# Optimization experiments

Hardware: AMD Instinct MI355X
Metric: run time of the kernel (lower is better)

## Reference

```python
import jax, jax.numpy as jnp
import numpy as np

ALPHA_MGD = 2e-05
NOISE_SIGMA = 8.0
NOISE_VAR = NOISE_SIGMA ** 2  # 64.0


def _conv2d(x, w, b, pad):
    # x: [N,C,H,W], w: [O,I,kh,kw]
    y = jax.lax.conv_general_dilated(
        x, w, window_strides=(1, 1), padding=[(pad, pad), (pad, pad)],
        dimension_numbers=("NCHW", "OIHW", "NCHW"))
    return y + b[None, :, None, None]


def setup_inputs() -> dict:
    key = jax.random.key(0)
    ks = jax.random.split(key, 8)
    N, Cs, Ct, H, W = 8, 128, 256, 64, 64
    return {
        "preds_S": jax.random.normal(ks[0], (N, Cs, H, W), jnp.float32),
        "preds_T": jax.random.normal(ks[1], (N, Ct, H, W), jnp.float32),
        "W_align": jax.random.normal(ks[2], (Ct, Cs, 1, 1), jnp.float32) * 0.05,
        "b_align": jnp.zeros((Ct,), jnp.float32),
        "W_gen1": jax.random.normal(ks[3], (Ct, Ct, 3, 3), jnp.float32) * 0.02,
        "b_gen1": jnp.zeros((Ct,), jnp.float32),
        "W_gen2": jax.random.normal(ks[4], (Ct, Ct, 3, 3), jnp.float32) * 0.02,
        "b_gen2": jnp.zeros((Ct,), jnp.float32),
    }


def reference(preds_S, preds_T, W_align, b_align, W_gen1, b_gen1, W_gen2, b_gen2):
    # align student channels to teacher channels (1x1 conv)
    s = _conv2d(preds_S, W_align, b_align, pad=0)
    N, C, H, W = preds_T.shape
    # deterministic checkerboard mask: tile([[0,1],[1,0]]) cropped to HxW -> (h+w) % 2
    hh = jnp.arange(H)[:, None]
    ww = jnp.arange(W)[None, :]
    mat = ((hh + ww) % 2).astype(s.dtype)  # [H,W]
    masked_fea = s * mat  # broadcast over [N,C,H,W]
    # generation network: conv3x3 -> relu -> conv3x3
    new_fea = _conv2d(jax.nn.relu(_conv2d(masked_fea, W_gen1, b_gen1, pad=1)), W_gen2, b_gen2, pad=1)
    # bmc_loss_md(pred=preds_T, target=new_fea, noise_var=64):
    # logits[i,j] = MVN(pred_i, noise_var*I).log_prob(target_j); the normalization
    # constant is class-independent and cancels in cross-entropy, keep the quadratic term.
    p = preds_T.reshape(N, -1)   # [N, D], D = C*H*W
    t = new_fea.reshape(N, -1)   # [N, D]
    # pairwise squared L2 via ||p||^2 + ||t||^2 - 2 p.t  (avoids NxNxD blow-up)
    sq = (jnp.sum(p * p, axis=1)[:, None]
          + jnp.sum(t * t, axis=1)[None, :]
          - 2.0 * (p @ t.T))  # [N, N]
    logits = -0.5 * sq / NOISE_VAR
    # cross_entropy(logits, arange(N)) = mean_i (logsumexp_j logits[i,j] - logits[i,i])
    ce = jnp.mean(jax.nn.logsumexp(logits, axis=1) - jnp.diagonal(logits))
    loss = ce * (2.0 * NOISE_VAR) / N
    return loss * ALPHA_MGD
```

## Files before the change

### kernel.cpp

```cpp
#include <hip/hip_runtime.h>

typedef unsigned short u16;
typedef short short8 __attribute__((ext_vector_type(8)));
typedef unsigned short ushort8 __attribute__((ext_vector_type(8)));
typedef float floatx16 __attribute__((ext_vector_type(16)));

#define PLANE8   34848
#define NSTRIDE  1115136

__device__ __forceinline__ u16 f2b(float f) {
  unsigned u = __builtin_bit_cast(unsigned, f);
  return (u16)((u + 0x7FFFu + ((u >> 16) & 1u)) >> 16);
}
__device__ __forceinline__ float b2f(u16 b) {
  return __builtin_bit_cast(float, ((unsigned)b) << 16);
}

typedef const __attribute__((address_space(1))) unsigned int* gptr_t;
typedef __attribute__((address_space(3))) unsigned int* sptr_t;

__global__ __launch_bounds__(256) void kprep(
    const float* __restrict__ Wg1, u16* __restrict__ Wsw1,
    const float* __restrict__ Wg2, u16* __restrict__ Wsw2,
    const float* __restrict__ Wa,  u16* __restrict__ Wb,
    const float* __restrict__ pS,  u16* __restrict__ T,
    u16* __restrict__ masked, u16* __restrict__ t1)
{
  __shared__ u16 Ls[64 * 136];
  int b = blockIdx.x, t = threadIdx.x;

  if (b < 576) {
    const float* W = (b < 288) ? Wg1 : Wg2;
    u16* D = (b < 288) ? Wsw1 : Wsw2;
    int bb = (b < 288) ? b : b - 288;
    int cid = bb * 256 + t;
    int d = cid % 1152, ctcg = cid / 1152;
    int ct = ctcg & 3, cg = ctcg >> 2;
    int colow = d & 31, cihalf = (d >> 5) & 1, sc = (d >> 6) & 1, tap = d >> 7;
    int co = ct * 64 + sc * 32 + colow;
    short8 v;
    #pragma unroll
    for (int jj = 0; jj < 8; ++jj) {
      int ci = cg * 16 + cihalf * 8 + jj;
      v[jj] = (short)f2b(W[((size_t)(co * 256 + ci)) * 9 + tap]);
    }
    *(short8*)&D[(size_t)cid * 8] = v;
  } else if (b < 592) {
    int v = (b - 576) * 256 + t;
    int colow = v & 31, hfb = (v >> 5) & 1, cog = (v >> 6) & 7, k = v >> 9;
    int co = cog * 32 + colow;
    int ci0 = k * 16 + hfb * 8;
    float4 f0 = *(const float4*)(Wa + (size_t)co * 128 + ci0);
    float4 f1 = *(const float4*)(Wa + (size_t)co * 128 + ci0 + 4);
    short8 o;
    o[0] = (short)f2b(f0.x); o[1] = (short)f2b(f0.y);
    o[2] = (short)f2b(f0.z); o[3] = (short)f2b(f0.w);
    o[4] = (short)f2b(f1.x); o[5] = (short)f2b(f1.y);
    o[6] = (short)f2b(f1.z); o[7] = (short)f2b(f1.w);
    *(short8*)&Wb[(size_t)v * 8] = o;
  } else if (b < 1104) {
    int bb = b - 592;
    int n = bb >> 6, pt = bb & 63, pix0 = pt * 64;
    int ci = t >> 1, ph = t & 1;
    const float* src = pS + ((size_t)n * 128 + ci) * 4096 + pix0 + ph * 32;
    #pragma unroll
    for (int i = 0; i < 8; ++i) {
      float4 v4 = *(const float4*)(src + i * 4);
      int pix = ph * 32 + i * 4;
      Ls[(pix + 0) * 136 + ci] = f2b(v4.x);
      Ls[(pix + 1) * 136 + ci] = f2b(v4.y);
      Ls[(pix + 2) * 136 + ci] = f2b(v4.z);
      Ls[(pix + 3) * 136 + ci] = f2b(v4.w);
    }
    __syncthreads();
    int p = t >> 2, q = t & 3;
    const u16* row = Ls + p * 136 + q * 32;
    u16* dst = T + ((size_t)n * 4096 + pix0 + p) * 128 + q * 32;
    #pragma unroll
    for (int k2 = 0; k2 < 4; ++k2)
      *(ushort8*)(dst + k2 * 8) = *(const ushort8*)(row + k2 * 8);
  } else {
    int p = b - 1104;
    u16* base = ((p >> 8) ? t1 : masked);
    int q = p & 255;
    base += (size_t)(q >> 5) * NSTRIDE + (size_t)(q & 31) * PLANE8;
    short8 z;
    #pragma unroll
    for (int jj = 0; jj < 8; ++jj) z[jj] = 0;
    #pragma unroll
    for (int pass = 0; pass < 2; ++pass) {
      int seg = t + pass * 256;
      if (seg < 264) {
        int off;
        if (seg < 66)       off = seg * 8;
        else if (seg < 132) off = (65 * 66 + (seg - 66)) * 8;
        else if (seg < 198) off = ((seg - 132) * 66) * 8;
        else                off = ((seg - 198) * 66 + 65) * 8;
        *(short8*)(base + off) = z;
      }
    }
  }
}

__global__ __launch_bounds__(256) void k1m(const u16* __restrict__ T,
    const u16* __restrict__ Wb, const float* __restrict__ ba,
    u16* __restrict__ mk)
{
  __shared__ __align__(16) u16 Wl[32768];
  int b = blockIdx.x;
  int n = b >> 5, pt = b & 31;
  int t = threadIdx.x, wid = t >> 6, lane = t & 63;
  int ml = lane & 31, hf = lane >> 5;

  #pragma unroll
  for (int kk = 0; kk < 16; ++kk) {
    int chunk = kk * 256 + t;
    __builtin_amdgcn_global_load_lds((gptr_t)(const void*)(Wb + (size_t)chunk * 8),
                                     (sptr_t)(void*)(Wl + chunk * 8), 16, 0, 0);
  }

  const u16* Tn = T + (size_t)n * 524288;
  const u16* ap[4];
  #pragma unroll
  for (int g = 0; g < 4; ++g)
    ap[g] = Tn + (size_t)(pt * 128 + g * 32 + ml) * 128 + hf * 8;

  floatx16 acc[2][4];
  #pragma unroll
  for (int q = 0; q < 2; ++q)
    #pragma unroll
    for (int g = 0; g < 4; ++g)
      #pragma unroll
      for (int i = 0; i < 16; ++i) acc[q][g][i] = 0.f;

  __syncthreads();

  const short8* WlV = (const short8*)Wl;
  int cogb = wid * 2;

  short8 a0[4], a1[4];
  #pragma unroll
  for (int g = 0; g < 4; ++g) a0[g] = *(const short8*)(ap[g]);

#define K1M_STEP(K, CUR, NXT, LAST)                                           \
  {                                                                           \
    if (!(LAST)) {                                                            \
      _Pragma("unroll")                                                       \
      for (int g = 0; g < 4; ++g)                                             \
        NXT[g] = *(const short8*)(ap[g] + ((K) + 1) * 16);                    \
    }                                                                         \
    short8 w0 = WlV[((K) * 8 + cogb) * 64 + lane];                            \
    short8 w1 = WlV[((K) * 8 + cogb + 1) * 64 + lane];                        \
    _Pragma("unroll")                                                         \
    for (int g = 0; g < 4; ++g) {                                             \
      acc[0][g] = __builtin_amdgcn_mfma_f32_32x32x16_bf16(CUR[g], w0, acc[0][g], 0, 0, 0); \
      acc[1][g] = __builtin_amdgcn_mfma_f32_32x32x16_bf16(CUR[g], w1, acc[1][g], 0, 0, 0); \
    }                                                                         \
  }
  K1M_STEP(0, a0, a1, 0)
  K1M_STEP(1, a1, a0, 0)
  K1M_STEP(2, a0, a1, 0)
  K1M_STEP(3, a1, a0, 0)
  K1M_STEP(4, a0, a1, 0)
  K1M_STEP(5, a1, a0, 0)
  K1M_STEP(6, a0, a1, 0)
  K1M_STEP(7, a1, a0, 1)
#undef K1M_STEP

  int co0 = cogb * 32 + ml, co1 = co0 + 32;
  float b0 = ba[co0], b1 = ba[co1];
  u16* base0 = mk + (size_t)n * NSTRIDE + (size_t)(co0 >> 3) * PLANE8 + (co0 & 7);
  u16* base1 = mk + (size_t)n * NSTRIDE + (size_t)(co1 >> 3) * PLANE8 + (co1 & 7);
  #pragma unroll
  for (int g = 0; g < 4; ++g)
    #pragma unroll
    for (int reg = 0; reg < 16; ++reg) {
      int m = (reg & 3) + 8 * (reg >> 2) + 4 * hf;
      int pix = pt * 128 + g * 32 + m;
      int h = pix >> 6, w = pix & 63;
      float msk = (float)((h + w) & 1);
      int off = ((h + 1) * 66 + (w + 1)) * 8;
      base0[off] = f2b((acc[0][g][reg] + b0) * msk);
      base1[off] = f2b((acc[1][g][reg] + b1) * msk);
    }
}

template <int MODE>
__global__ __launch_bounds__(128) void kconv(
    const u16* __restrict__ IN, const u16* __restrict__ WS,
    const float* __restrict__ bg, u16* __restrict__ OUT)
{
  __shared__ __align__(16) u16 LinA[896 * 8];
  __shared__ __align__(16) u16 LinB[896 * 8];
  __shared__ __align__(16) u16 LwA[1152 * 8];
  __shared__ __align__(16) u16 LwB[1152 * 8];

  int b = blockIdx.x;
  int rt = b & 15, ct = (b >> 4) & 3, n = b >> 6;
  int h0 = rt * 4;
  int t = threadIdx.x;
  int wid = t >> 6, lane = t & 63;
  int hf = lane >> 5, ml = lane & 31;

  int in_goff[7];
  int lds_off[7];
  #pragma unroll
  for (int k = 0; k < 7; ++k) {
    int seg = 2 * k + wid;
    int half = seg >= 7 ? 1 : 0;
    int s = seg - half * 7;
    in_goff[k] = half * PLANE8 + (h0 * 66 + s * 64 + lane) * 8;
    lds_off[k] = (half * 448 + s * 64) * 8;
  }

  const u16* inb = IN + (size_t)n * NSTRIDE;
  const u16* wg  = WS + (size_t)ct * 1152 * 8;

  floatx16 acc[2][2][2];
  #pragma unroll
  for (int r = 0; r < 2; ++r)
    #pragma unroll
    for (int s = 0; s < 2; ++s)
      #pragma unroll
      for (int q = 0; q < 2; ++q)
        #pragma unroll
        for (int i = 0; i < 16; ++i) acc[r][s][q][i] = 0.f;

  auto STAGE = [&](int cg, u16* LinD, u16* LwD) {
    #pragma unroll
    for (int k = 0; k < 9; ++k) {
      int sidx = wid + 2 * k;
      const u16* src = wg + (size_t)cg * 36864 + (size_t)(sidx * 64 + lane) * 8;
      __builtin_amdgcn_global_load_lds((gptr_t)(const void*)src,
                                       (sptr_t)(void*)(LwD + sidx * 512), 16, 0, 0);
    }
    #pragma unroll
    for (int k = 0; k < 7; ++k) {
      const u16* src = inb + (size_t)cg * 69696 + in_goff[k];
      __builtin_amdgcn_global_load_lds((gptr_t)(const void*)src,
                                       (sptr_t)(void*)(LinD + lds_off[k]), 16, 0, 0);
    }
  };

  auto COMPUTE = [&](const u16* LinS, const u16* LwS) {
    const short8* LinV = (const short8*)LinS;
    const short8* LwV  = (const short8*)LwS;
    int rb = hf * 448 + 2 * wid * 66;
    #pragma unroll
    for (int dc = 0; dc < 3; ++dc) {
      short8 ifr[4][2];
      #pragma unroll
      for (int rr = 0; rr < 4; ++rr) {
        ifr[rr][0] = LinV[rb + rr * 66 + ml + dc];
        ifr[rr][1] = LinV[rb + rr * 66 + 32 + ml + dc];
      }
      #pragma unroll
      for (int dr = 0; dr < 3; ++dr) {
        int tap = dr * 3 + dc;
        short8 w0 = LwV[tap * 128 + lane];
        short8 w1 = LwV[tap * 128 + 64 + lane];
        acc[0][0][0] = __builtin_amdgcn_mfma_f32_32x32x16_bf16(ifr[dr][0],     w0, acc[0][0][0], 0, 0, 0);
        acc[0][0][1] = __builtin_amdgcn_mfma_f32_32x32x16_bf16(ifr[dr][0],     w1, acc[0][0][1], 0, 0, 0);
        acc[0][1][0] = __builtin_amdgcn_mfma_f32_32x32x16_bf16(ifr[dr][1],     w0, acc[0][1][0], 0, 0, 0);
        acc[0][1][1] = __builtin_amdgcn_mfma_f32_32x32x16_bf16(ifr[dr][1],     w1, acc[0][1][1], 0, 0, 0);
        acc[1][0][0] = __builtin_amdgcn_mfma_f32_32x32x16_bf16(ifr[dr + 1][0], w0, acc[1][0][0], 0, 0, 0);
        acc[1][0][1] = __builtin_amdgcn_mfma_f32_32x32x16_bf16(ifr[dr + 1][0], w1, acc[1][0][1], 0, 0, 0);
        acc[1][1][0] = __builtin_amdgcn_mfma_f32_32x32x16_bf16(ifr[dr + 1][1], w0, acc[1][1][0], 0, 0, 0);
        acc[1][1][1] = __builtin_amdgcn_mfma_f32_32x32x16_bf16(ifr[dr + 1][1], w1, acc[1][1][1], 0, 0, 0);
      }
    }
  };

  STAGE(0, LinA, LwA);
  __syncthreads();
  for (int cg = 0; cg < 16; cg += 2) {
    STAGE(cg + 1, LinB, LwB);
    COMPUTE(LinA, LwA);
    __syncthreads();
    if (cg + 2 < 16) STAGE(cg + 2, LinA, LwA);
    COMPUTE(LinB, LwB);
    __syncthreads();
  }

  float bias0 = bg[ct * 64 + ml];
  float bias1 = bg[ct * 64 + 32 + ml];

  if (MODE == 0) {
    u16* ob = OUT + (size_t)n * NSTRIDE;
    int co0 = ct * 64 + ml, co1 = co0 + 32;
    int cb0 = ((co0 >> 4) * 2 + ((co0 >> 3) & 1)) * PLANE8 + (co0 & 7);
    int cb1 = ((co1 >> 4) * 2 + ((co1 >> 3) & 1)) * PLANE8 + (co1 & 7);
    #pragma unroll
    for (int r = 0; r < 2; ++r) {
      int rowoff = (h0 + 2 * wid + r + 1) * 66 + 1;
      #pragma unroll
      for (int reg = 0; reg < 16; ++reg) {
        int m = (reg & 3) + 8 * (reg >> 2) + 4 * hf;
        float v;
        v = acc[r][0][0][reg] + bias0; v = fmaxf(v, 0.f); ob[cb0 + (rowoff + m) * 8] = f2b(v);
        v = acc[r][0][1][reg] + bias1; v = fmaxf(v, 0.f); ob[cb1 + (rowoff + m) * 8] = f2b(v);
        v = acc[r][1][0][reg] + bias0; v = fmaxf(v, 0.f); ob[cb0 + (rowoff + 32 + m) * 8] = f2b(v);
        v = acc[r][1][1][reg] + bias1; v = fmaxf(v, 0.f); ob[cb1 + (rowoff + 32 + m) * 8] = f2b(v);
      }
    }
  } else {
    u16* plane = (wid == 0) ? LinA : LwA;
    #pragma unroll
    for (int r = 0; r < 2; ++r) {
      __syncthreads();
      #pragma unroll
      for (int reg = 0; reg < 16; ++reg) {
        int m = (reg & 3) + 8 * (reg >> 2) + 4 * hf;
        plane[ml * 68 + m]              = f2b(acc[r][0][0][reg] + bias0);
        plane[(32 + ml) * 68 + m]       = f2b(acc[r][0][1][reg] + bias1);
        plane[ml * 68 + 32 + m]         = f2b(acc[r][1][0][reg] + bias0);
        plane[(32 + ml) * 68 + 32 + m]  = f2b(acc[r][1][1][reg] + bias1);
      }
      __syncthreads();
      const u16* row = plane + lane * 68;
      __align__(16) u16 tmp[64];
      #pragma unroll
      for (int k2 = 0; k2 < 16; ++k2)
        *(ushort4*)(tmp + k2 * 4) = *(const ushort4*)(row + k2 * 4);
      u16* gdst = OUT + (size_t)n * 1048576 + (size_t)(ct * 64 + lane) * 4096
                  + (h0 + 2 * wid + r) * 64;
      #pragma unroll
      for (int k2 = 0; k2 < 8; ++k2)
        *(ushort8*)(gdst + k2 * 8) = *(const ushort8*)(tmp + k2 * 8);
    }
  }
}

__global__ __launch_bounds__(256) void kbmc(const u16* __restrict__ t2,
    const float* __restrict__ pT, float* __restrict__ part)
{
  int t = threadIdx.x, lane = t & 63, role = t >> 6;
  int ih = role >> 1, nh = role & 1;
  int bid = blockIdx.x;

  float pt[4][4], pp[4], tt[4];
  #pragma unroll
  for (int i = 0; i < 4; ++i) {
    pp[i] = 0.f; tt[i] = 0.f;
    #pragma unroll
    for (int j = 0; j < 4; ++j) pt[i][j] = 0.f;
  }

  const float* pb = pT + ((size_t)ih * 4) * 1048576;
  const u16*   tb = t2 + ((size_t)nh * 4) * 1048576;

  for (int k = 0; k < 8; ++k) {
    size_t d0 = ((size_t)(bid * 512 + k * 64 + lane)) * 4;
    float4 p[4], tf[4];
    #pragma unroll
    for (int i = 0; i < 4; ++i)
      p[i] = *(const float4*)(pb + (size_t)i * 1048576 + d0);
    #pragma unroll
    for (int j = 0; j < 4; ++j) {
      ushort4 tv = *(const ushort4*)(tb + (size_t)j * 1048576 + d0);
      tf[j] = make_float4(b2f(tv.x), b2f(tv.y), b2f(tv.z), b2f(tv.w));
    }
    if (nh == 0) {
      #pragma unroll
      for (int i = 0; i < 4; ++i)
        pp[i] += p[i].x * p[i].x + p[i].y * p[i].y + p[i].z * p[i].z + p[i].w * p[i].w;
    }
    if (ih == 0) {
      #pragma unroll
      for (int j = 0; j < 4; ++j)
        tt[j] += tf[j].x * tf[j].x + tf[j].y * tf[j].y + tf[j].z * tf[j].z + tf[j].w * tf[j].w;
    }
    #pragma unroll
    for (int i = 0; i < 4; ++i)
      #pragma unroll
      for (int j = 0; j < 4; ++j)
        pt[i][j] += p[i].x * tf[j].x + p[i].y * tf[j].y
                  + p[i].z * tf[j].z + p[i].w * tf[j].w;
  }

  #pragma unroll
  for (int m = 1; m < 64; m <<= 1) {
    #pragma unroll
    for (int i = 0; i < 4; ++i) {
      pp[i] += __shfl_xor(pp[i], m);
      tt[i] += __shfl_xor(tt[i], m);
      #pragma unroll
      for (int j = 0; j < 4; ++j) pt[i][j] += __shfl_xor(pt[i][j], m);
    }
  }
  if (lane == 0) {
    #pragma unroll
    for (int i = 0; i < 4; ++i)
      #pragma unroll
      for (int j = 0; j < 4; ++j)
        part[(size_t)(16 + (ih * 4 + i) * 8 + (nh * 4 + j)) * 512 + bid] = pt[i][j];
    if (nh == 0) {
      #pragma unroll
      for (int i = 0; i < 4; ++i) part[(size_t)(ih * 4 + i) * 512 + bid] = pp[i];
    }
    if (ih == 0) {
      #pragma unroll
      for (int j = 0; j < 4; ++j) part[(size_t)(8 + nh * 4 + j) * 512 + bid] = tt[j];
    }
  }
}

__global__ __launch_bounds__(256) void kred(const float* __restrict__ part,
                                            float* __restrict__ accums)
{
  __shared__ float r4[4];
  int s = blockIdx.x, t = threadIdx.x, lane = t & 63, wid = t >> 6;
  float v = part[(size_t)s * 512 + t] + part[(size_t)s * 512 + 256 + t];
  #pragma unroll
  for (int m = 1; m < 64; m <<= 1) v += __shfl_xor(v, m);
  if (lane == 0) r4[wid] = v;
  __syncthreads();
  if (t == 0) accums[s] = r4[0] + r4[1] + r4[2] + r4[3];
}

__global__ void k4_final(const float* __restrict__ accums, float* __restrict__ out)
{
  int t = threadIdx.x;
  int i = t >> 3, j = t & 7;
  double pp = accums[i];
  double tt = accums[8 + j];
  double pt = accums[16 + i * 8 + j];
  double logit = -0.5 * (pp + tt - 2.0 * pt) / 64.0;
  double m = logit;
  #pragma unroll
  for (int s = 1; s < 8; s <<= 1) {
    double o = __shfl_xor(m, s);
    m = o > m ? o : m;
  }
  double e = exp(logit - m);
  #pragma unroll
  for (int s = 1; s < 8; s <<= 1) e += __shfl_xor(e, s);
  double lse = m + log(e);
  double term = (j == i) ? (lse - logit) : 0.0;
  #pragma unroll
  for (int s = 1; s < 64; s <<= 1) term += __shfl_xor(term, s);
  if (t == 0) {
    double ce = term / 8.0;
    out[0] = (float)(ce * (2.0 * 64.0) / 8.0 * 2e-05);
  }
}

extern "C" void kernel_launch(void* const* d_in, const int* in_sizes, int n_in,
                              void* d_out, int out_size, void* d_ws, size_t ws_size,
                              hipStream_t stream)
{
  const float* preds_S = (const float*)d_in[0];
  const float* preds_T = (const float*)d_in[1];
  const float* W_align = (const float*)d_in[2];
  const float* b_align = (const float*)d_in[3];
  const float* W_gen1  = (const float*)d_in[4];
  const float* b_gen1  = (const float*)d_in[5];
  const float* W_gen2  = (const float*)d_in[6];
  const float* b_gen2  = (const float*)d_in[7];
  float* out = (float*)d_out;

  char* wsb = (char*)d_ws;
  u16* masked = (u16*)wsb;
  u16* t1     = (u16*)(wsb + 17842176);
  u16* t2p    = (u16*)(wsb + 35684352);
  u16* T      = t2p;
  u16* Wsw1   = (u16*)(wsb + 52461568);
  u16* Wsw2   = (u16*)(wsb + 53641216);
  float* part   = (float*)(wsb + 54820864);
  float* accums = (float*)(wsb + 55017472);
  u16* Wb     = (u16*)(wsb + 55017856);

  kprep<<<1616, 256, 0, stream>>>(W_gen1, Wsw1, W_gen2, Wsw2, W_align, Wb,
                                  preds_S, T, masked, t1);
  k1m<<<256, 256, 0, stream>>>(T, Wb, b_align, masked);
  kconv<0><<<512, 128, 0, stream>>>(masked, Wsw1, b_gen1, t1);
  kconv<1><<<512, 128, 0, stream>>>(t1, Wsw2, b_gen2, t2p);
  kbmc<<<512, 256, 0, stream>>>(t2p, preds_T, part);
  kred<<<80, 256, 0, stream>>>(part, accums);
  k4_final<<<1, 64, 0, stream>>>(accums, out);
}
```

Baseline: 209.3 us.

## Use partial vmcnt waits and raw barriers to overlap LDS staging with MFMA

Replaces __syncthreads (which drains all outstanding global loads) with explicit s_waitcnt vmcnt(16)/lgkmcnt(0) plus s_barrier. The previous stage's loads can then complete while the next stage's 16 global_load_lds ops stay in flight during compute. Also raises wave priority around the MFMA block with s_setprio and peels the last iteration. The risk is that hand-counted vmcnt values must match the exact number of loads issued per stage (16), or the code reads stale LDS data.

```diff
diff --git a/kernel.cpp b/kernel.cpp
--- a/kernel.cpp
+++ b/kernel.cpp
@@ -246,6 +246,7 @@
     const short8* LinV = (const short8*)LinS;
     const short8* LwV  = (const short8*)LwS;
     int rb = hf * 448 + 2 * wid * 66;
+    __builtin_amdgcn_s_setprio(1);
     #pragma unroll
     for (int dc = 0; dc < 3; ++dc) {
       short8 ifr[4][2];
@@ -269,18 +270,42 @@
         acc[1][1][1] = __builtin_amdgcn_mfma_f32_32x32x16_bf16(ifr[dr + 1][1], w1, acc[1][1][1], 0, 0, 0);
       }
     }
+    __builtin_amdgcn_s_setprio(0);
   };
 
+#define WAIT_VM16() { asm volatile("s_waitcnt vmcnt(16)" ::: "memory"); \
+                      __builtin_amdgcn_sched_barrier(0); }
+#define WAIT_VM0()  { asm volatile("s_waitcnt vmcnt(0)" ::: "memory");  \
+                      __builtin_amdgcn_sched_barrier(0); }
+#define WAIT_LGKM0(){ asm volatile("s_waitcnt lgkmcnt(0)" ::: "memory"); \
+                      __builtin_amdgcn_sched_barrier(0); }
+#define BAR()       { __builtin_amdgcn_s_barrier(); \
+                      __builtin_amdgcn_sched_barrier(0); }
+
   STAGE(0, LinA, LwA);
-  __syncthreads();
-  for (int cg = 0; cg < 16; cg += 2) {
+  WAIT_VM0(); BAR();
+  for (int cg = 0; cg < 14; cg += 2) {
     STAGE(cg + 1, LinB, LwB);
+    WAIT_VM16(); BAR();
     COMPUTE(LinA, LwA);
-    __syncthreads();
-    if (cg + 2 < 16) STAGE(cg + 2, LinA, LwA);
+    WAIT_LGKM0(); BAR();
+    STAGE(cg + 2, LinA, LwA);
+    WAIT_VM16(); BAR();
     COMPUTE(LinB, LwB);
-    __syncthreads();
-  }
+    WAIT_LGKM0(); BAR();
+  }
+  STAGE(15, LinB, LwB);
+  WAIT_VM16(); BAR();
+  COMPUTE(LinA, LwA);
+  WAIT_LGKM0(); BAR();
+  WAIT_VM0(); BAR();
+  COMPUTE(LinB, LwB);
+  WAIT_LGKM0(); BAR();
+
+#undef WAIT_VM16
+#undef WAIT_VM0
+#undef WAIT_LGKM0
+#undef BAR
 
   float bias0 = bg[ct * 64 + ml];
   float bias1 = bg[ct * 64 + 32 + ml];
```

New measurement: 217.0 us. 1.04x slower.
